# Kernel tuning notes

Hardware: AMD Instinct MI355X
Metric: run time of the kernel (lower is better)

The kernel has to match this reference:

```python
import jax, jax.numpy as jnp
import numpy as np

B, T, D, H = 2, 2048, 1024, 8
HD = D // H

def setup_inputs() -> dict:
    key = jax.random.key(0)
    ks = jax.random.split(key, 6)
    s = 1.0 / np.sqrt(D)
    x = jax.random.normal(ks[0], (B, T, D), dtype=jnp.float32)
    Wq = jax.random.normal(ks[1], (D, D), dtype=jnp.float32) * s
    Wk = jax.random.normal(ks[2], (D, D), dtype=jnp.float32) * s
    Wv = jax.random.normal(ks[3], (D, D), dtype=jnp.float32) * s
    Wo = jax.random.normal(ks[4], (D, D), dtype=jnp.float32) * s
    bo = jnp.zeros((D,), dtype=jnp.float32)
    # theta[i] = 1 / 10000**(2i/H) as in _init_parameters
    theta = (1.0 / (10000.0 ** (2.0 * jnp.arange(H, dtype=jnp.float32) / H))).astype(jnp.float32)
    gamma = jnp.ones((D,), dtype=jnp.float32)   # group_norm weight
    beta = jnp.zeros((D,), dtype=jnp.float32)   # group_norm bias
    return {"x": x, "Wq": Wq, "Wk": Wk, "Wv": Wv, "Wo": Wo, "bo": bo,
            "theta": theta, "gamma": gamma, "beta": beta}

def reference(x, Wq, Wk, Wv, Wo, bo, theta, gamma, beta):
    b, t, d = x.shape
    h = theta.shape[0]
    hd = d // h
    q = (x @ Wq).reshape(b, t, h, hd)
    k = (x @ Wk).reshape(b, t, h, hd)
    v = (x @ Wv).reshape(b, t, h, hd)

    # decay mask: vectorized closed form of the O(T^2) python loop.
    # mask[i,j] = mean_h exp(-theta_h * (i-j)) for j<=i else 0
    pos = jnp.arange(t, dtype=jnp.float32)
    n = pos[:, None] - pos[None, :]                       # (T,T) i-j
    nn = jnp.maximum(n, 0.0)
    decay_mask = jnp.where(n >= 0,
                           jnp.mean(jnp.exp(-theta[None, None, :] * nn[:, :, None]), axis=-1),
                           0.0)                            # (T,T)

    scores = jnp.einsum('bthd,bshd->bths', q, k) / np.sqrt(hd)   # (B,T,H,T)
    scores = scores * decay_mask[None, :, None, :]
    causal = (n >= 0)[None, :, None, :]
    scores = jnp.where(causal, scores, -jnp.inf)
    retention = jax.nn.softmax(scores, axis=-1)
    out = jnp.einsum('bths,bshd->bthd', retention, v)            # (B,T,H,HD)

    # GroupNorm(num_heads, d_model): normalize each head's hd-chunk per token
    mu = out.mean(axis=-1, keepdims=True)
    var = out.var(axis=-1, keepdims=True)
    out = (out - mu) / jnp.sqrt(var + 1e-5)
    out = out.reshape(b, t, d) * gamma + beta

    return out @ Wo + bo
```

## Files before the change

### kernel.cpp

```cpp
#include <hip/hip_runtime.h>

#define B_SZ  2
#define T_SEQ 2048
#define D_MOD 1024
#define NH    8
#define HD    128

typedef __attribute__((ext_vector_type(8))) short short8;
typedef __attribute__((ext_vector_type(4))) float f32x4;

__device__ __forceinline__ short f2bf(float f) {
  unsigned u = __float_as_uint(f);
  unsigned r = u + 0x7fffu + ((u >> 16) & 1u);
  return (short)(r >> 16);
}

__device__ __forceinline__ void gld_lds16(const short* g, short* l) {
  __builtin_amdgcn_global_load_lds(
      (const __attribute__((address_space(1))) void*)g,
      (__attribute__((address_space(3))) void*)l, 16, 0, 0);
}

__global__ void decay_kernel(const float* __restrict__ theta,
                             float* __restrict__ dm) {
  int n = blockIdx.x * 256 + threadIdx.x;
  if (n >= T_SEQ) return;
  float nf = (float)n;
  float s = 0.f;
#pragma unroll
  for (int h = 0; h < NH; h++) s += __expf(-theta[h] * nf);
  dm[n] = s * (0.08838834764831845f / 8.0f);
}

__global__ __launch_bounds__(256) void cvt_x(const float* __restrict__ x,
                                             short* __restrict__ xb) {
  int i = (blockIdx.x * 256 + threadIdx.x) * 8;
  float4 a = *(const float4*)(x + i);
  float4 b = *(const float4*)(x + i + 4);
  short8 o;
  o[0] = f2bf(a.x); o[1] = f2bf(a.y); o[2] = f2bf(a.z); o[3] = f2bf(a.w);
  o[4] = f2bf(b.x); o[5] = f2bf(b.y); o[6] = f2bf(b.z); o[7] = f2bf(b.w);
  *(short8*)(xb + i) = o;
}

__global__ __launch_bounds__(256) void cvt_w(const float* __restrict__ Wq,
                                             const float* __restrict__ Wk,
                                             const float* __restrict__ Wv,
                                             const float* __restrict__ Wo,
                                             short* __restrict__ wt) {
  __shared__ float t[32][33];
  const int z = blockIdx.z;
  const float* __restrict__ W = (z == 0) ? Wq : (z == 1) ? Wk : (z == 2) ? Wv : Wo;
  short* __restrict__ dst = wt + (size_t)z * D_MOD * D_MOD;
  const int k0 = blockIdx.x * 32, n0 = blockIdx.y * 32;
  const int tx = threadIdx.x & 31, ty = threadIdx.x >> 5;
#pragma unroll
  for (int i = 0; i < 4; i++)
    t[ty * 4 + i][tx] = W[(size_t)(k0 + ty * 4 + i) * D_MOD + n0 + tx];
  __syncthreads();
#pragma unroll
  for (int i = 0; i < 4; i++)
    dst[(size_t)(n0 + ty * 4 + i) * D_MOD + k0 + tx] = f2bf(t[tx][ty * 4 + i]);
}

__global__ __launch_bounds__(256, 3) void gemm_qkv(
    const short* __restrict__ xb, const short* __restrict__ wt,
    short* __restrict__ qb, short* __restrict__ kb, short* __restrict__ vb) {
  __shared__ __align__(16) short As[128 * 32];
  __shared__ __align__(16) short Bs[128 * 32];
  const int tid = threadIdx.x;
  const int l = tid & 63, w = tid >> 6;
  const int wr = w >> 1, wc = w & 1;
  const int row0 = blockIdx.x * 128;
  const int h = blockIdx.y;
  const int col0 = h * 128;
  const short* __restrict__ Wt = wt + (size_t)blockIdx.z * D_MOD * D_MOD;
  short* __restrict__ dst = (blockIdx.z == 0) ? qb : (blockIdx.z == 1) ? kb : vb;

  f32x4 acc[4][4];
#pragma unroll
  for (int m = 0; m < 4; m++)
#pragma unroll
    for (int n = 0; n < 4; n++) acc[m][n] = (f32x4){0.f, 0.f, 0.f, 0.f};

  const int cA = w * 2;
  const int sr = l >> 2;
  const int skq = (l & 3) << 3;

#pragma unroll
  for (int i = 0; i < 2; i++) {
    int c = cA + i;
    gld_lds16(xb + (size_t)(row0 + c * 16 + sr) * D_MOD + skq, As + c * 512);
    gld_lds16(Wt + (size_t)(col0 + c * 16 + sr) * D_MOD + skq, Bs + c * 512);
  }
  for (int ks = 0; ks < 32; ks++) {
    __syncthreads();
    short8 af[4], bf[4];
#pragma unroll
    for (int m = 0; m < 4; m++)
      af[m] = *(const short8*)&As[(wr * 64 + m * 16 + (l & 15)) * 32 + (l >> 4) * 8];
#pragma unroll
    for (int n = 0; n < 4; n++)
      bf[n] = *(const short8*)&Bs[(wc * 64 + n * 16 + (l & 15)) * 32 + (l >> 4) * 8];
#pragma unroll
    for (int m = 0; m < 4; m++)
#pragma unroll
      for (int n = 0; n < 4; n++)
        acc[m][n] =
            __builtin_amdgcn_mfma_f32_16x16x32_bf16(af[m], bf[n], acc[m][n], 0, 0, 0);
    __syncthreads();
    if (ks < 31) {
      const int k0 = (ks + 1) * 32;
#pragma unroll
      for (int i = 0; i < 2; i++) {
        int c = cA + i;
        gld_lds16(xb + (size_t)(row0 + c * 16 + sr) * D_MOD + k0 + skq, As + c * 512);
        gld_lds16(Wt + (size_t)(col0 + c * 16 + sr) * D_MOD + k0 + skq, Bs + c * 512);
      }
    }
  }
#pragma unroll
  for (int m = 0; m < 4; m++) {
#pragma unroll
    for (int j = 0; j < 4; j++) {
      int row = row0 + wr * 64 + m * 16 + (l >> 4) * 4 + j;
      int bb = row >> 11, t = row & (T_SEQ - 1);
      size_t base = ((size_t)(bb * NH + h) * T_SEQ + t) * HD + wc * 64 + (l & 15);
#pragma unroll
      for (int n = 0; n < 4; n++) dst[base + n * 16] = f2bf(acc[m][n][j]);
    }
  }
}

__global__ __launch_bounds__(256, 3) void gemm_out(
    const short* __restrict__ yb, const short* __restrict__ wot,
    const float* __restrict__ bias, float* __restrict__ out) {
  __shared__ __align__(16) short As[128 * 32];
  __shared__ __align__(16) short Bs[128 * 32];
  const int tid = threadIdx.x;
  const int l = tid & 63, w = tid >> 6;
  const int wr = w >> 1, wc = w & 1;
  const int row0 = blockIdx.x * 128;
  const int col0 = blockIdx.y * 128;

  f32x4 acc[4][4];
#pragma unroll
  for (int m = 0; m < 4; m++)
#pragma unroll
    for (int n = 0; n < 4; n++) acc[m][n] = (f32x4){0.f, 0.f, 0.f, 0.f};

  const int cA = w * 2;
  const int sr = l >> 2;
  const int skq = (l & 3) << 3;

#pragma unroll
  for (int i = 0; i < 2; i++) {
    int c = cA + i;
    gld_lds16(yb + (size_t)(row0 + c * 16 + sr) * D_MOD + skq, As + c * 512);
    gld_lds16(wot + (size_t)(col0 + c * 16 + sr) * D_MOD + skq, Bs + c * 512);
  }
  for (int ks = 0; ks < 32; ks++) {
    __syncthreads();
    short8 af[4], bf[4];
#pragma unroll
    for (int m = 0; m < 4; m++)
      af[m] = *(const short8*)&As[(wr * 64 + m * 16 + (l & 15)) * 32 + (l >> 4) * 8];
#pragma unroll
    for (int n = 0; n < 4; n++)
      bf[n] = *(const short8*)&Bs[(wc * 64 + n * 16 + (l & 15)) * 32 + (l >> 4) * 8];
#pragma unroll
    for (int m = 0; m < 4; m++)
#pragma unroll
      for (int n = 0; n < 4; n++)
        acc[m][n] =
            __builtin_amdgcn_mfma_f32_16x16x32_bf16(af[m], bf[n], acc[m][n], 0, 0, 0);
    __syncthreads();
    if (ks < 31) {
      const int k0 = (ks + 1) * 32;
#pragma unroll
      for (int i = 0; i < 2; i++) {
        int c = cA + i;
        gld_lds16(yb + (size_t)(row0 + c * 16 + sr) * D_MOD + k0 + skq, As + c * 512);
        gld_lds16(wot + (size_t)(col0 + c * 16 + sr) * D_MOD + k0 + skq, Bs + c * 512);
      }
    }
  }
#pragma unroll
  for (int m = 0; m < 4; m++) {
#pragma unroll
    for (int j = 0; j < 4; j++) {
      int row = row0 + wr * 64 + m * 16 + (l >> 4) * 4 + j;
#pragma unroll
      for (int n = 0; n < 4; n++) {
        int col = col0 + wc * 64 + n * 16 + (l & 15);
        out[(size_t)row * D_MOD + col] = acc[m][n][j] + bias[col];
      }
    }
  }
}

__global__ __launch_bounds__(256, 2) void attn_kernel(
    const short* __restrict__ qg, const short* __restrict__ kg,
    const short* __restrict__ vg, const float* __restrict__ dm_g,
    const float* __restrict__ gamma, const float* __restrict__ beta,
    short* __restrict__ yb) {
  __shared__ __align__(16) short KT[2][8192];
  __shared__ __align__(16) short VT[2][8192];
  __shared__ float dm_s[T_SEQ];

  const int tid = threadIdx.x;
  const int l = tid & 63, w = tid >> 6;
  const int lm = l & 15, lq = l >> 4;

  const unsigned pbid = blockIdx.x;
  const unsigned lbid = (pbid & 7) * 64 + (pbid >> 3);
  const int qraw = lbid & 31;
  const int qt = (lbid & 32) ? (31 - qraw) : qraw;
  const int h = (lbid >> 5) & 7;
  const int b = lbid >> 8;

  const size_t hoff = (size_t)(b * NH + h) * T_SEQ * HD;
  const short* __restrict__ Qh = qg + hoff;
  const short* __restrict__ Kh = kg + hoff;
  const short* __restrict__ Vh = vg + hoff;

  for (int i = tid * 4; i < T_SEQ; i += 1024)
    *(float4*)&dm_s[i] = *(const float4*)&dm_g[i];

  short8 qf[4];
  {
    int row = qt * 64 + w * 16 + lm;
#pragma unroll
    for (int kc = 0; kc < 4; kc++)
      qf[kc] = *(const short8*)(Qh + (size_t)row * HD + kc * 32 + lq * 8);
  }

  f32x4 zero4 = {0.f, 0.f, 0.f, 0.f};
  f32x4 o[8];
#pragma unroll
  for (int cb = 0; cb < 8; cb++) o[cb] = zero4;
  float m_r = -1e30f, l_r = 0.f;

  const int i_row = qt * 64 + w * 16 + lm;
  const int d0 = l * 2;
  const int srcA = lm + 32 * (lq & 1);
  const int srcB = srcA + 16;
  unsigned vv[16];

  {
    const int jP = qt * 64;
#pragma unroll
    for (int kc = 0; kc < 4; kc++)
      gld_lds16(Kh + (size_t)(jP + w * 16 + lm) * HD + kc * 32 + lq * 8,
                &KT[0][(w * 4 + kc) * 512]);
#pragma unroll
    for (int p = 0; p < 2; p++)
#pragma unroll
      for (int jj = 0; jj < 8; jj++)
        vv[p * 8 + jj] =
            *(const unsigned*)(Vh + (size_t)(jP + (w + p * 4) * 8 + jj) * HD + d0);
#pragma unroll
    for (int p = 0; p < 2; p++) {
      const int jl = (w + p * 4) * 8;
      const int kc2 = jl >> 5, bq = (jl >> 3) & 3;
#pragma unroll
      for (int dd = 0; dd < 2; dd++) {
        const int d = d0 + dd;
        short8 col;
#pragma unroll
        for (int jj = 0; jj < 8; jj++) {
          unsigned u = vv[p * 8 + jj];
          col[jj] = (short)(dd ? (u >> 16) : (u & 0xffffu));
        }
        *(short8*)&VT[0][(((d >> 4) * 2 + kc2) * 64 + bq * 16 + (d & 15)) * 8] = col;
      }
    }
  }
  __syncthreads();

  int cur = 0;
  for (int t = qt; t >= 0; --t) {
    const int j0 = t * 64;
    const int nxt = cur ^ 1;
    const bool pf = (t > 0);

    if (pf) {
      const int jn = j0 - 64;
#pragma unroll
      for (int kc = 0; kc < 4; kc++)
        gld_lds16(Kh + (size_t)(jn + w * 16 + lm) * HD + kc * 32 + lq * 8,
                  &KT[nxt][(w * 4 + kc) * 512]);
#pragma unroll
      for (int p = 0; p < 2; p++)
#pragma unroll
        for (int jj = 0; jj < 8; jj++)
          vv[p * 8 + jj] =
              *(const unsigned*)(Vh + (size_t)(jn + (w + p * 4) * 8 + jj) * HD + d0);
    }

    short8 kfr[16];
#pragma unroll
    for (int jb = 0; jb < 4; jb++)
#pragma unroll
      for (int kc = 0; kc < 4; kc++)
        kfr[jb * 4 + kc] = *(const short8*)&KT[cur][((jb * 4 + kc) * 64 + l) * 8];

    float s[4][4];
    __builtin_amdgcn_s_setprio(1);
#pragma unroll
    for (int jb = 0; jb < 4; jb++) {
      f32x4 acc = zero4;
#pragma unroll
      for (int kc = 0; kc < 4; kc++)
        acc = __builtin_amdgcn_mfma_f32_16x16x32_bf16(kfr[jb * 4 + kc], qf[kc],
                                                      acc, 0, 0, 0);
#pragma unroll
      for (int r = 0; r < 4; r++) {
        int delta = i_row - (j0 + jb * 16 + lq * 4 + r);
        float sv = acc[r] * dm_s[delta & (T_SEQ - 1)];
        s[jb][r] = (delta >= 0) ? sv : -__builtin_inff();
      }
    }
    __builtin_amdgcn_s_setprio(0);

    short8 vfr[16];
#pragma unroll
    for (int cb = 0; cb < 8; cb++)
#pragma unroll
      for (int kc2 = 0; kc2 < 2; kc2++)
        vfr[cb * 2 + kc2] =
            *(const short8*)&VT[cur][((cb * 2 + kc2) * 64 + l) * 8];

    float lmax = fmaxf(fmaxf(fmaxf(s[0][0], s[0][1]), fmaxf(s[0][2], s[0][3])),
                       fmaxf(fmaxf(s[1][0], s[1][1]), fmaxf(s[1][2], s[1][3])));
    lmax = fmaxf(lmax,
                 fmaxf(fmaxf(fmaxf(s[2][0], s[2][1]), fmaxf(s[2][2], s[2][3])),
                       fmaxf(fmaxf(s[3][0], s[3][1]), fmaxf(s[3][2], s[3][3]))));
    if (__any(lmax > m_r + 4.0f)) {
      float mx = lmax;
      mx = fmaxf(mx, __shfl_xor(mx, 16));
      mx = fmaxf(mx, __shfl_xor(mx, 32));
      float mnew = fmaxf(m_r, mx);
      float fac = __expf(m_r - mnew);
      m_r = mnew;
      l_r *= fac;
      float facr[4];
#pragma unroll
      for (int r = 0; r < 4; r++) facr[r] = __shfl(fac, lq * 4 + r);
#pragma unroll
      for (int cb = 0; cb < 8; cb++)
#pragma unroll
        for (int r = 0; r < 4; r++) o[cb][r] *= facr[r];
    }

    float lsum = 0.f;
#pragma unroll
    for (int jb = 0; jb < 4; jb++)
#pragma unroll
      for (int r = 0; r < 4; r++) {
        float pv = __expf(s[jb][r] - m_r);
        s[jb][r] = pv;
        lsum += pv;
      }
    lsum += __shfl_xor(lsum, 16);
    lsum += __shfl_xor(lsum, 32);
    l_r += lsum;

    unsigned pw[4][2];
#pragma unroll
    for (int jb = 0; jb < 4; jb++) {
      asm("v_cvt_pk_bf16_f32 %0, %1, %2"
          : "=v"(pw[jb][0]) : "v"(s[jb][0]), "v"(s[jb][1]));
      asm("v_cvt_pk_bf16_f32 %0, %1, %2"
          : "=v"(pw[jb][1]) : "v"(s[jb][2]), "v"(s[jb][3]));
    }

    __builtin_amdgcn_s_setprio(1);
#pragma unroll
    for (int kc2 = 0; kc2 < 2; kc2++) {
      unsigned w0a = __shfl((int)pw[2 * kc2][0], srcA);
      unsigned w0b = __shfl((int)pw[2 * kc2 + 1][0], srcA);
      unsigned w1a = __shfl((int)pw[2 * kc2][1], srcA);
      unsigned w1b = __shfl((int)pw[2 * kc2 + 1][1], srcA);
      unsigned w2a = __shfl((int)pw[2 * kc2][0], srcB);
      unsigned w2b = __shfl((int)pw[2 * kc2 + 1][0], srcB);
      unsigned w3a = __shfl((int)pw[2 * kc2][1], srcB);
      unsigned w3b = __shfl((int)pw[2 * kc2 + 1][1], srcB);
      const bool hi = (lq & 2) != 0;
      unsigned w0 = hi ? w0b : w0a;
      unsigned w1 = hi ? w1b : w1a;
      unsigned w2 = hi ? w2b : w2a;
      unsigned w3 = hi ? w3b : w3a;
      short8 pb;
      pb[0] = (short)(w0 & 0xffffu); pb[1] = (short)(w0 >> 16);
      pb[2] = (short)(w1 & 0xffffu); pb[3] = (short)(w1 >> 16);
      pb[4] = (short)(w2 & 0xffffu); pb[5] = (short)(w2 >> 16);
      pb[6] = (short)(w3 & 0xffffu); pb[7] = (short)(w3 >> 16);
#pragma unroll
      for (int cb = 0; cb < 8; cb++)
        o[cb] = __builtin_amdgcn_mfma_f32_16x16x32_bf16(pb, vfr[cb * 2 + kc2],
                                                        o[cb], 0, 0, 0);
    }
    __builtin_amdgcn_s_setprio(0);

    if (pf) {
#pragma unroll
      for (int p = 0; p < 2; p++) {
        const int jl = (w + p * 4) * 8;
        const int kc2 = jl >> 5, bq = (jl >> 3) & 3;
#pragma unroll
        for (int dd = 0; dd < 2; dd++) {
          const int d = d0 + dd;
          short8 col;
#pragma unroll
          for (int jj = 0; jj < 8; jj++) {
            unsigned u = vv[p * 8 + jj];
            col[jj] = (short)(dd ? (u >> 16) : (u & 0xffffu));
          }
          *(short8*)&VT[nxt][(((d >> 4) * 2 + kc2) * 64 + bq * 16 + (d & 15)) * 8] =
              col;
        }
      }
    }
    __syncthreads();
    cur = nxt;
  }

  float linv[4];
#pragma unroll
  for (int r = 0; r < 4; r++) linv[r] = 1.0f / __shfl(l_r, lq * 4 + r);
  float mu[4], rstd[4];
#pragma unroll
  for (int r = 0; r < 4; r++) {
    float sum = 0.f, sq = 0.f;
#pragma unroll
    for (int cb = 0; cb < 8; cb++) {
      float v2 = o[cb][r] * linv[r];
      o[cb][r] = v2;
      sum += v2;
      sq += v2 * v2;
    }
    sum += __shfl_xor(sum, 1); sum += __shfl_xor(sum, 2);
    sum += __shfl_xor(sum, 4); sum += __shfl_xor(sum, 8);
    sq += __shfl_xor(sq, 1); sq += __shfl_xor(sq, 2);
    sq += __shfl_xor(sq, 4); sq += __shfl_xor(sq, 8);
    float m2 = sum * (1.f / 128.f);
    mu[r] = m2;
    rstd[r] = rsqrtf(sq * (1.f / 128.f) - m2 * m2 + 1e-5f);
  }
  const int trow = qt * 64 + w * 16 + lq * 4;
#pragma unroll
  for (int cb = 0; cb < 8; cb++) {
    const int dcol = h * HD + cb * 16 + lm;
    const float g = gamma[dcol], be = beta[dcol];
#pragma unroll
    for (int r = 0; r < 4; r++) {
      float val = (o[cb][r] - mu[r]) * rstd[r] * g + be;
      yb[(size_t)(b * T_SEQ + trow + r) * D_MOD + dcol] = f2bf(val);
    }
  }
}

extern "C" void kernel_launch(void* const* d_in, const int* in_sizes, int n_in,
                              void* d_out, int out_size, void* d_ws,
                              size_t ws_size, hipStream_t stream) {
  const float* x     = (const float*)d_in[0];
  const float* Wq    = (const float*)d_in[1];
  const float* Wk    = (const float*)d_in[2];
  const float* Wv    = (const float*)d_in[3];
  const float* Wo    = (const float*)d_in[4];
  const float* bo    = (const float*)d_in[5];
  const float* theta = (const float*)d_in[6];
  const float* gamma = (const float*)d_in[7];
  const float* beta  = (const float*)d_in[8];
  float* out = (float*)d_out;

  char* ws = (char*)d_ws;
  const size_t MB = 1024 * 1024;
  short* qb = (short*)(ws + 0 * MB);
  short* kb = (short*)(ws + 8 * MB);
  short* vb = (short*)(ws + 16 * MB);
  short* yb = (short*)(ws + 24 * MB);
  short* xb = (short*)(ws + 32 * MB);
  short* wt = (short*)(ws + 40 * MB);
  float* dm = (float*)(ws + 48 * MB);

  decay_kernel<<<dim3(8), dim3(256), 0, stream>>>(theta, dm);
  cvt_x<<<dim3(2048), dim3(256), 0, stream>>>(x, xb);
  cvt_w<<<dim3(32, 32, 4), dim3(256), 0, stream>>>(Wq, Wk, Wv, Wo, wt);
  gemm_qkv<<<dim3(32, 8, 3), dim3(256), 0, stream>>>(xb, wt, qb, kb, vb);
  attn_kernel<<<dim3(512), dim3(256), 0, stream>>>(qb, kb, vb, dm, gamma, beta, yb);
  gemm_out<<<dim3(32, 8), dim3(256), 0, stream>>>(
      yb, wt + (size_t)3 * D_MOD * D_MOD, bo, out);
}
```

Measured before the change: 211.2 us.

## Halve attention KV tile to 32 keys and raise occupancy to four blocks per CU

```diff
diff --git a/kernel.cpp b/kernel.cpp
--- a/kernel.cpp
+++ b/kernel.cpp
@@ -199,13 +199,13 @@
   }
 }
 
-__global__ __launch_bounds__(256, 2) void attn_kernel(
+__global__ __launch_bounds__(256, 4) void attn_kernel(
     const short* __restrict__ qg, const short* __restrict__ kg,
     const short* __restrict__ vg, const float* __restrict__ dm_g,
     const float* __restrict__ gamma, const float* __restrict__ beta,
     short* __restrict__ yb) {
-  __shared__ __align__(16) short KT[2][8192];
-  __shared__ __align__(16) short VT[2][8192];
+  __shared__ __align__(16) short KT[2][4096];
+  __shared__ __align__(16) short VT[2][4096];
   __shared__ float dm_s[T_SEQ];
 
   const int tid = threadIdx.x;
@@ -245,70 +245,64 @@
   const int d0 = l * 2;
   const int srcA = lm + 32 * (lq & 1);
   const int srcB = srcA + 16;
-  unsigned vv[16];
+  const int tmax = 2 * qt + 1;
+  unsigned vv[8];
 
   {
-    const int jP = qt * 64;
-#pragma unroll
-    for (int kc = 0; kc < 4; kc++)
-      gld_lds16(Kh + (size_t)(jP + w * 16 + lm) * HD + kc * 32 + lq * 8,
-                &KT[0][(w * 4 + kc) * 512]);
-#pragma unroll
-    for (int p = 0; p < 2; p++)
-#pragma unroll
-      for (int jj = 0; jj < 8; jj++)
-        vv[p * 8 + jj] =
-            *(const unsigned*)(Vh + (size_t)(jP + (w + p * 4) * 8 + jj) * HD + d0);
-#pragma unroll
-    for (int p = 0; p < 2; p++) {
-      const int jl = (w + p * 4) * 8;
-      const int kc2 = jl >> 5, bq = (jl >> 3) & 3;
-#pragma unroll
-      for (int dd = 0; dd < 2; dd++) {
-        const int d = d0 + dd;
-        short8 col;
-#pragma unroll
-        for (int jj = 0; jj < 8; jj++) {
-          unsigned u = vv[p * 8 + jj];
-          col[jj] = (short)(dd ? (u >> 16) : (u & 0xffffu));
-        }
-        *(short8*)&VT[0][(((d >> 4) * 2 + kc2) * 64 + bq * 16 + (d & 15)) * 8] = col;
-      }
+    const int jP = tmax * 32;
+#pragma unroll
+    for (int i = 0; i < 2; i++) {
+      const int c = w * 2 + i;
+      gld_lds16(Kh + (size_t)(jP + (c >> 2) * 16 + lm) * HD + (c & 3) * 32 + lq * 8,
+                &KT[0][c * 512]);
+    }
+#pragma unroll
+    for (int jj = 0; jj < 8; jj++)
+      vv[jj] = *(const unsigned*)(Vh + (size_t)(jP + w * 8 + jj) * HD + d0);
+#pragma unroll
+    for (int dd = 0; dd < 2; dd++) {
+      const int d = d0 + dd;
+      short8 col;
+#pragma unroll
+      for (int jj = 0; jj < 8; jj++) {
+        unsigned u = vv[jj];
+        col[jj] = (short)(dd ? (u >> 16) : (u & 0xffffu));
+      }
+      *(short8*)&VT[0][(((d >> 4) * 64) + w * 16 + (d & 15)) * 8] = col;
     }
   }
   __syncthreads();
 
   int cur = 0;
-  for (int t = qt; t >= 0; --t) {
-    const int j0 = t * 64;
+  for (int t = tmax; t >= 0; --t) {
+    const int j0 = t * 32;
     const int nxt = cur ^ 1;
     const bool pf = (t > 0);
 
     if (pf) {
-      const int jn = j0 - 64;
-#pragma unroll
-      for (int kc = 0; kc < 4; kc++)
-        gld_lds16(Kh + (size_t)(jn + w * 16 + lm) * HD + kc * 32 + lq * 8,
-                  &KT[nxt][(w * 4 + kc) * 512]);
-#pragma unroll
-      for (int p = 0; p < 2; p++)
-#pragma unroll
-        for (int jj = 0; jj < 8; jj++)
-          vv[p * 8 + jj] =
-              *(const unsigned*)(Vh + (size_t)(jn + (w + p * 4) * 8 + jj) * HD + d0);
-    }
-
-    short8 kfr[16];
-#pragma unroll
-    for (int jb = 0; jb < 4; jb++)
+      const int jn = j0 - 32;
+#pragma unroll
+      for (int i = 0; i < 2; i++) {
+        const int c = w * 2 + i;
+        gld_lds16(Kh + (size_t)(jn + (c >> 2) * 16 + lm) * HD + (c & 3) * 32 + lq * 8,
+                  &KT[nxt][c * 512]);
+      }
+#pragma unroll
+      for (int jj = 0; jj < 8; jj++)
+        vv[jj] = *(const unsigned*)(Vh + (size_t)(jn + w * 8 + jj) * HD + d0);
+    }
+
+    short8 kfr[8];
+#pragma unroll
+    for (int jb = 0; jb < 2; jb++)
 #pragma unroll
       for (int kc = 0; kc < 4; kc++)
         kfr[jb * 4 + kc] = *(const short8*)&KT[cur][((jb * 4 + kc) * 64 + l) * 8];
 
-    float s[4][4];
+    float s[2][4];
     __builtin_amdgcn_s_setprio(1);
 #pragma unroll
-    for (int jb = 0; jb < 4; jb++) {
+    for (int jb = 0; jb < 2; jb++) {
       f32x4 acc = zero4;
 #pragma unroll
       for (int kc = 0; kc < 4; kc++)
@@ -323,19 +317,13 @@
     }
     __builtin_amdgcn_s_setprio(0);
 
-    short8 vfr[16];
+    short8 vfr[8];
 #pragma unroll
     for (int cb = 0; cb < 8; cb++)
-#pragma unroll
-      for (int kc2 = 0; kc2 < 2; kc2++)
-        vfr[cb * 2 + kc2] =
-            *(const short8*)&VT[cur][((cb * 2 + kc2) * 64 + l) * 8];
+      vfr[cb] = *(const short8*)&VT[cur][(cb * 64 + l) * 8];
 
     float lmax = fmaxf(fmaxf(fmaxf(s[0][0], s[0][1]), fmaxf(s[0][2], s[0][3])),
                        fmaxf(fmaxf(s[1][0], s[1][1]), fmaxf(s[1][2], s[1][3])));
-    lmax = fmaxf(lmax,
-                 fmaxf(fmaxf(fmaxf(s[2][0], s[2][1]), fmaxf(s[2][2], s[2][3])),
-                       fmaxf(fmaxf(s[3][0], s[3][1]), fmaxf(s[3][2], s[3][3]))));
     if (__any(lmax > m_r + 4.0f)) {
       float mx = lmax;
       mx = fmaxf(mx, __shfl_xor(mx, 16));
@@ -355,7 +343,7 @@
 
     float lsum = 0.f;
 #pragma unroll
-    for (int jb = 0; jb < 4; jb++)
+    for (int jb = 0; jb < 2; jb++)
 #pragma unroll
       for (int r = 0; r < 4; r++) {
         float pv = __expf(s[jb][r] - m_r);
@@ -366,9 +354,9 @@
     lsum += __shfl_xor(lsum, 32);
     l_r += lsum;
 
-    unsigned pw[4][2];
-#pragma unroll
-    for (int jb = 0; jb < 4; jb++) {
+    unsigned pw[2][2];
+#pragma unroll
+    for (int jb = 0; jb < 2; jb++) {
       asm("v_cvt_pk_bf16_f32 %0, %1, %2"
           : "=v"(pw[jb][0]) : "v"(s[jb][0]), "v"(s[jb][1]));
       asm("v_cvt_pk_bf16_f32 %0, %1, %2"
@@ -376,16 +364,15 @@
     }
 
     __builtin_amdgcn_s_setprio(1);
-#pragma unroll
-    for (int kc2 = 0; kc2 < 2; kc2++) {
-      unsigned w0a = __shfl((int)pw[2 * kc2][0], srcA);
-      unsigned w0b = __shfl((int)pw[2 * kc2 + 1][0], srcA);
-      unsigned w1a = __shfl((int)pw[2 * kc2][1], srcA);
-      unsigned w1b = __shfl((int)pw[2 * kc2 + 1][1], srcA);
-      unsigned w2a = __shfl((int)pw[2 * kc2][0], srcB);
-      unsigned w2b = __shfl((int)pw[2 * kc2 + 1][0], srcB);
-      unsigned w3a = __shfl((int)pw[2 * kc2][1], srcB);
-      unsigned w3b = __shfl((int)pw[2 * kc2 + 1][1], srcB);
+    {
+      unsigned w0a = __shfl((int)pw[0][0], srcA);
+      unsigned w0b = __shfl((int)pw[1][0], srcA);
+      unsigned w1a = __shfl((int)pw[0][1], srcA);
+      unsigned w1b = __shfl((int)pw[1][1], srcA);
+      unsigned w2a = __shfl((int)pw[0][0], srcB);
+      unsigned w2b = __shfl((int)pw[1][0], srcB);
+      unsigned w3a = __shfl((int)pw[0][1], srcB);
+      unsigned w3b = __shfl((int)pw[1][1], srcB);
       const bool hi = (lq & 2) != 0;
       unsigned w0 = hi ? w0b : w0a;
       unsigned w1 = hi ? w1b : w1a;
@@ -398,28 +385,22 @@
       pb[6] = (short)(w3 & 0xffffu); pb[7] = (short)(w3 >> 16);
 #pragma unroll
       for (int cb = 0; cb < 8; cb++)
-        o[cb] = __builtin_amdgcn_mfma_f32_16x16x32_bf16(pb, vfr[cb * 2 + kc2],
-                                                        o[cb], 0, 0, 0);
+        o[cb] = __builtin_amdgcn_mfma_f32_16x16x32_bf16(pb, vfr[cb], o[cb],
+                                                        0, 0, 0);
     }
     __builtin_amdgcn_s_setprio(0);
 
     if (pf) {
 #pragma unroll
-      for (int p = 0; p < 2; p++) {
-        const int jl = (w + p * 4) * 8;
-        const int kc2 = jl >> 5, bq = (jl >> 3) & 3;
-#pragma unroll
-        for (int dd = 0; dd < 2; dd++) {
-          const int d = d0 + dd;
-          short8 col;
-#pragma unroll
-          for (int jj = 0; jj < 8; jj++) {
-            unsigned u = vv[p * 8 + jj];
-            col[jj] = (short)(dd ? (u >> 16) : (u & 0xffffu));
-          }
-          *(short8*)&VT[nxt][(((d >> 4) * 2 + kc2) * 64 + bq * 16 + (d & 15)) * 8] =
-              col;
+      for (int dd = 0; dd < 2; dd++) {
+        const int d = d0 + dd;
+        short8 col;
+#pragma unroll
+        for (int jj = 0; jj < 8; jj++) {
+          unsigned u = vv[jj];
+          col[jj] = (short)(dd ? (u >> 16) : (u & 0xffffu));
         }
+        *(short8*)&VT[nxt][(((d >> 4) * 64) + w * 16 + (d & 15)) * 8] = col;
       }
     }
     __syncthreads();
```

After: 217.2 us. +2.8%, slower.
